# Kernel optimization log

Hardware: AMD Instinct MI355X
Metric: run time of the kernel (lower is better)

The kernel has to match this reference:

```python
import jax, jax.numpy as jnp
import numpy as np

EPS = 1e-6
B, N, WD, R = 64, 1024, 64, 4
IN_DIM, HID, OUT_DIM = 512, 512, 256


def oneplus(x):
    return 1.0 + jax.nn.softplus(x)


def content_weight(M, keys, strengths):
    # M:[B,N,W] keys:[B,R,W] strengths:[B,R] -> softmax over N -> [B,N,R]
    Mn = M * jax.lax.rsqrt(jnp.sum(M * M, -1, keepdims=True) + EPS)
    kn = keys * jax.lax.rsqrt(jnp.sum(keys * keys, -1, keepdims=True) + EPS)
    sim = jnp.einsum('bnw,brw->bnr', Mn, kn)
    return jax.nn.softmax(sim * strengths[:, None, :], axis=1)


def allocation(u):
    # DNC allocation weighting: sort usage ascending, exclusive cumprod, scatter back
    idx = jnp.argsort(u, axis=-1)
    us = jnp.take_along_axis(u, idx, -1)
    cp = jnp.cumprod(us, -1)
    cp_excl = jnp.concatenate([jnp.ones_like(cp[:, :1]), cp[:, :-1]], -1)
    a_sorted = (1.0 - us) * cp_excl
    inv = jnp.argsort(idx, axis=-1)
    return jnp.take_along_axis(a_sorted, inv, -1)


def setup_inputs() -> dict:
    key = jax.random.key(0)
    ks = jax.random.split(key, 16)
    rw = jax.random.uniform(ks[0], (B, N, R), dtype=jnp.float32)
    rw = rw / jnp.sum(rw, axis=1, keepdims=True)  # valid read distribution over N
    wwp = jax.random.uniform(ks[1], (B, N), dtype=jnp.float32)
    wwp = wwp / jnp.sum(wwp, axis=1, keepdims=True)
    s = 0.02
    return {
        'x': jax.random.normal(ks[2], (B, IN_DIM), dtype=jnp.float32),
        'read_weighting': rw,
        'memory': jax.random.normal(ks[3], (B, N, WD), dtype=jnp.float32) * 0.1,
        'usage': jax.random.uniform(ks[4], (B, N), dtype=jnp.float32),
        'write_weighting_prev': wwp,
        'link': jnp.zeros((B, N, N), dtype=jnp.float32),
        'precedence': jnp.zeros((B, N), dtype=jnp.float32),
        'W1': jax.random.normal(ks[5], (IN_DIM + R * WD, HID), dtype=jnp.float32) * s,
        'b1': jnp.zeros((HID,), dtype=jnp.float32),
        'Wo': jax.random.normal(ks[6], (HID, OUT_DIM), dtype=jnp.float32) * s,
        'bo': jnp.zeros((OUT_DIM,), dtype=jnp.float32),
        'Wr': jax.random.normal(ks[7], (R * WD, OUT_DIM), dtype=jnp.float32) * s,
        'br': jnp.zeros((OUT_DIM,), dtype=jnp.float32),
        'Wxi': jax.random.normal(ks[8], (HID, WD * R + 3 * WD + 5 * R + 3), dtype=jnp.float32) * s,
        'bxi': jnp.zeros((WD * R + 3 * WD + 5 * R + 3,), dtype=jnp.float32),
    }


def reference(x, read_weighting, memory, usage, write_weighting_prev, link, precedence,
              W1, b1, Wo, bo, Wr, br, Wxi, bxi):
    b, n, wd = memory.shape
    r = read_weighting.shape[-1]
    # --- read with incoming read weighting ---
    read_flat = jnp.einsum('bnw,bnr->brw', memory, read_weighting).reshape(b, r * wd)
    h = jax.nn.relu(jnp.concatenate([x, read_flat], -1) @ W1 + b1)
    output = (h @ Wo + bo) + (read_flat @ Wr + br)
    xi = h @ Wxi + bxi
    # --- interface split ---
    sizes = [wd * r, r, wd, 1, wd, wd, r, 1, 1, 3 * r]
    offs = np.cumsum([0] + sizes)
    p = [xi[:, offs[i]:offs[i + 1]] for i in range(10)]
    read_keys = p[0].reshape(b, r, wd)
    read_strengths = oneplus(p[1])
    write_key = p[2][:, None, :]
    write_strength = oneplus(p[3])
    erase = jax.nn.sigmoid(p[4])
    write_vec = p[5]
    free = jax.nn.sigmoid(p[6])
    ag = jax.nn.sigmoid(p[7])
    wg = jax.nn.sigmoid(p[8])
    read_modes = jax.nn.softmax(p[9].reshape(b, r, 3), axis=-1)
    # --- dynamic memory allocation ---
    retention = jnp.prod(1.0 - free[:, None, :] * read_weighting, axis=-1)  # [B,N]
    usage_new = (usage + write_weighting_prev - usage * write_weighting_prev) * retention
    alloc = allocation(usage_new)
    wc = content_weight(memory, write_key, write_strength)[:, :, 0]
    ww = wg * (ag * alloc + (1.0 - ag) * wc)  # [B,N]
    # --- erase / write ---
    memory_new = memory * (1.0 - ww[:, :, None] * erase[:, None, :]) \
        + ww[:, :, None] * write_vec[:, None, :]
    # --- temporal link matrix ---
    prec_new = (1.0 - jnp.sum(ww, -1, keepdims=True)) * precedence + ww
    link_new = (1.0 - ww[:, :, None] - ww[:, None, :]) * link \
        + ww[:, :, None] * precedence[:, None, :]
    link_new = link_new * (1.0 - jnp.eye(n, dtype=link.dtype))
    fwd_w = jnp.einsum('bij,bjr->bir', link_new, read_weighting)
    bwd_w = jnp.einsum('bji,bjr->bir', link_new, read_weighting)
    # --- new read weighting ---
    cr = content_weight(memory_new, read_keys, read_strengths)
    rw_new = read_modes[:, None, :, 0] * bwd_w \
        + read_modes[:, None, :, 1] * cr \
        + read_modes[:, None, :, 2] * fwd_w
    return output, xi, rw_new, memory_new, usage_new
```

## Files before the change

### kernel.cpp

```cpp
#include <hip/hip_runtime.h>

#define NB 64
#define NN 1024
#define WDIM 64
#define RR 4
#define HID 512
#define XID 471
#define EPSF 1e-6f

#define O_OUT   0
#define O_XI    16384
#define O_RW    46528
#define O_MEM   308672
#define O_USAGE 4502976

#define WS_RFPART   0
#define WS_H        65536
#define WS_IFACE    98304
#define WS_ALLOC    129024
#define WS_WW       194560
#define WS_V        260096
#define WS_DIAG     784896
#define WS_ROWAB    850432
#define WS_COLPART  1899008
#define WS_EW       6093312
#define WS_SIMWE    6093568
#define WS_ERP      6159104
#define WS_ER       6160128
#define WS_STP      6422272

#define IF_KN     0
#define IF_WKN    256
#define IF_ERASE  320
#define IF_WVEC   384
#define IF_RSTR   448
#define IF_FREE   452
#define IF_WSTR   456
#define IF_AG     457
#define IF_WG     458
#define IF_MODES  460
#define IF_STRIDE 480

__device__ __forceinline__ float sigmoidf_(float x) { return 1.0f / (1.0f + expf(-x)); }
__device__ __forceinline__ float oneplusf_(float x) {
  return 1.0f + ((x > 20.0f) ? x : log1pf(expf(x)));
}

typedef const __attribute__((address_space(1))) void gas_void;
typedef __attribute__((address_space(3))) void las_void;
__device__ __forceinline__ void gl16(const float* g, float* l) {
  __builtin_amdgcn_global_load_lds((gas_void*)g, (las_void*)l, 16, 0, 0);
}

__global__ __launch_bounds__(1024) void k_read_flat(const float* __restrict__ mem,
                                                    const float* __restrict__ rw,
                                                    float* __restrict__ ws) {
  __shared__ float red[1024];
  const int q = blockIdx.x, b = blockIdx.y, t = threadIdx.x;
  const int rwi = t & 255;
  const int r = rwi >> 6, w = rwi & 63;
  const int ng = t >> 8;
  const int n0 = (q << 8) + (ng << 6);
  const float* M  = mem + ((size_t)(b << 10) + n0) * WDIM;
  const float* Rw = rw  + ((size_t)(b << 10) + n0) * RR;
  float a0 = 0.f, a1 = 0.f, a2 = 0.f, a3 = 0.f;
  for (int n = 0; n < 64; n += 4) {
    a0 += M[(n + 0) * WDIM + w] * Rw[(n + 0) * RR + r];
    a1 += M[(n + 1) * WDIM + w] * Rw[(n + 1) * RR + r];
    a2 += M[(n + 2) * WDIM + w] * Rw[(n + 2) * RR + r];
    a3 += M[(n + 3) * WDIM + w] * Rw[(n + 3) * RR + r];
  }
  red[t] = (a0 + a1) + (a2 + a3);
  __syncthreads();
  if (t < 256)
    ws[WS_RFPART + (((q << 6) + b) << 8) + t] =
        red[t] + red[t + 256] + red[t + 512] + red[t + 768];
}

__global__ __launch_bounds__(256) void k_h(const float* __restrict__ x,
                                           const float* __restrict__ W1,
                                           const float* __restrict__ b1,
                                           float* __restrict__ ws) {
  __shared__ float cat[768];
  const int ch = blockIdx.x, b = blockIdx.y, t = threadIdx.x;
  cat[t] = x[b * 512 + t];
  cat[256 + t] = x[b * 512 + 256 + t];
  {
    float s = 0.0f;
    #pragma unroll
    for (int q = 0; q < 4; ++q) s += ws[WS_RFPART + (((q << 6) + b) << 8) + t];
    cat[512 + t] = s;
  }
  __syncthreads();
  const int col = (ch << 8) + t;
  float a0 = 0.f, a1 = 0.f, a2 = 0.f, a3 = 0.f;
  #pragma unroll 4
  for (int k = 0; k < 768; k += 4) {
    a0 = fmaf(cat[k + 0], W1[(k + 0) * 512 + col], a0);
    a1 = fmaf(cat[k + 1], W1[(k + 1) * 512 + col], a1);
    a2 = fmaf(cat[k + 2], W1[(k + 2) * 512 + col], a2);
    a3 = fmaf(cat[k + 3], W1[(k + 3) * 512 + col], a3);
  }
  ws[WS_H + b * 512 + col] = fmaxf(b1[col] + (a0 + a1) + (a2 + a3), 0.0f);
}

__global__ __launch_bounds__(256) void k_xiout(const float* __restrict__ Wxi,
                                               const float* __restrict__ bxi,
                                               const float* __restrict__ Wo,
                                               const float* __restrict__ bo,
                                               const float* __restrict__ Wr,
                                               const float* __restrict__ br,
                                               const float* __restrict__ ws,
                                               float* __restrict__ out) {
  __shared__ float h[512];
  __shared__ float rf[256];
  const int m = blockIdx.x, b = blockIdx.y, t = threadIdx.x;
  h[t] = ws[WS_H + b * 512 + t];
  h[256 + t] = ws[WS_H + b * 512 + 256 + t];
  if (m == 2) {
    float s = 0.0f;
    #pragma unroll
    for (int q = 0; q < 4; ++q) s += ws[WS_RFPART + (((q << 6) + b) << 8) + t];
    rf[t] = s;
  }
  __syncthreads();
  if (m < 2) {
    const int col = (m << 8) + t;
    if (col < XID) {
      float a0 = 0.f, a1 = 0.f, a2 = 0.f, a3 = 0.f;
      #pragma unroll 4
      for (int j = 0; j < 512; j += 4) {
        a0 = fmaf(h[j + 0], Wxi[(j + 0) * XID + col], a0);
        a1 = fmaf(h[j + 1], Wxi[(j + 1) * XID + col], a1);
        a2 = fmaf(h[j + 2], Wxi[(j + 2) * XID + col], a2);
        a3 = fmaf(h[j + 3], Wxi[(j + 3) * XID + col], a3);
      }
      out[O_XI + b * XID + col] = bxi[col] + (a0 + a1) + (a2 + a3);
    }
  } else {
    float a0 = 0.f, a1 = 0.f, a2 = 0.f, a3 = 0.f;
    #pragma unroll 4
    for (int j = 0; j < 512; j += 4) {
      a0 = fmaf(h[j + 0], Wo[(j + 0) * 256 + t], a0);
      a1 = fmaf(h[j + 1], Wo[(j + 1) * 256 + t], a1);
      a2 = fmaf(h[j + 2], Wo[(j + 2) * 256 + t], a2);
      a3 = fmaf(h[j + 3], Wo[(j + 3) * 256 + t], a3);
    }
    #pragma unroll 4
    for (int j = 0; j < 256; j += 4) {
      a0 = fmaf(rf[j + 0], Wr[(j + 0) * 256 + t], a0);
      a1 = fmaf(rf[j + 1], Wr[(j + 1) * 256 + t], a1);
      a2 = fmaf(rf[j + 2], Wr[(j + 2) * 256 + t], a2);
      a3 = fmaf(rf[j + 3], Wr[(j + 3) * 256 + t], a3);
    }
    out[O_OUT + b * 256 + t] = bo[t] + br[t] + (a0 + a1) + (a2 + a3);
  }
}

__global__ __launch_bounds__(64) void k_iface(const float* __restrict__ out,
                                              float* __restrict__ ws) {
  const int b = blockIdx.x, w = threadIdx.x;
  const float* xi = out + O_XI + b * XID;
  float* f = ws + WS_IFACE + (size_t)b * IF_STRIDE;
  #pragma unroll
  for (int r = 0; r < 4; ++r) {
    float kv = xi[r * 64 + w];
    float ss = kv * kv;
    #pragma unroll
    for (int s = 32; s; s >>= 1) ss += __shfl_xor(ss, s);
    f[IF_KN + r * 64 + w] = kv * rsqrtf(ss + EPSF);
  }
  {
    float kv = xi[260 + w];
    float ss = kv * kv;
    #pragma unroll
    for (int s = 32; s; s >>= 1) ss += __shfl_xor(ss, s);
    f[IF_WKN + w] = kv * rsqrtf(ss + EPSF);
  }
  f[IF_ERASE + w] = sigmoidf_(xi[325 + w]);
  f[IF_WVEC + w] = xi[389 + w];
  if (w < 4) {
    f[IF_RSTR + w] = oneplusf_(xi[256 + w]);
    f[IF_FREE + w] = sigmoidf_(xi[453 + w]);
    float a = xi[459 + w * 3], bb = xi[459 + w * 3 + 1], c = xi[459 + w * 3 + 2];
    float m = fmaxf(a, fmaxf(bb, c));
    float ea = expf(a - m), eb = expf(bb - m), ec = expf(c - m);
    float s = ea + eb + ec;
    f[IF_MODES + w * 3] = ea / s;
    f[IF_MODES + w * 3 + 1] = eb / s;
    f[IF_MODES + w * 3 + 2] = ec / s;
  }
  if (w == 0) {
    f[IF_WSTR] = oneplusf_(xi[324]);
    f[IF_AG] = sigmoidf_(xi[457]);
    f[IF_WG] = sigmoidf_(xi[458]);
  }
}

__global__ __launch_bounds__(256) void k_alloc(const float* __restrict__ rw,
                                               const float* __restrict__ usage,
                                               const float* __restrict__ wwp,
                                               float* __restrict__ ws,
                                               float* __restrict__ ousage) {
  __shared__ float2 ul[1024];
  const int q = blockIdx.x, b = blockIdx.y, t = threadIdx.x;
  const float* fr = ws + WS_IFACE + (size_t)b * IF_STRIDE + IF_FREE;
  const float f0 = fr[0], f1 = fr[1], f2 = fr[2], f3 = fr[3];
  #pragma unroll
  for (int c = 0; c < 4; ++c) {
    const int n = (c << 8) + t;
    const int i = (b << 10) + n;
    const float4 r4 = *(const float4*)(rw + (size_t)i * 4);
    float ret = (1.0f - f0 * r4.x) * (1.0f - f1 * r4.y) *
                (1.0f - f2 * r4.z) * (1.0f - f3 * r4.w);
    float u = usage[i], w = wwp[i];
    float un = (u + w - u * w) * ret;
    if (c == q) ousage[i] = un;
    ul[n] = make_float2(un, logf(un));
  }
  __syncthreads();
  const int i = (q << 8) + t;
  const float ui = ul[i].x;
  float s0 = 0.f, s1 = 0.f, s2 = 0.f, s3 = 0.f;
  #pragma unroll 2
  for (int j = 0; j < 1024; j += 4) {
    float2 v0 = ul[j], v1 = ul[j + 1], v2 = ul[j + 2], v3 = ul[j + 3];
    s0 += ((v0.x < ui) || (v0.x == ui && j + 0 < i)) ? v0.y : 0.0f;
    s1 += ((v1.x < ui) || (v1.x == ui && j + 1 < i)) ? v1.y : 0.0f;
    s2 += ((v2.x < ui) || (v2.x == ui && j + 2 < i)) ? v2.y : 0.0f;
    s3 += ((v3.x < ui) || (v3.x == ui && j + 3 < i)) ? v3.y : 0.0f;
  }
  ws[WS_ALLOC + (b << 10) + i] = (1.0f - ui) * expf((s0 + s1) + (s2 + s3));
}

__global__ __launch_bounds__(256) void k_wcww_a(const float* __restrict__ mem,
                                                const float* __restrict__ link,
                                                float* __restrict__ ws) {
  __shared__ float wkn[64];
  __shared__ float red[4];
  const int q = blockIdx.x, b = blockIdx.y, t = threadIdx.x;
  const int wv = t >> 6, lane = t & 63;
  const float* f = ws + WS_IFACE + (size_t)b * IF_STRIDE;
  if (t < 64) wkn[t] = f[IF_WKN + t];
  __syncthreads();
  const int n = (q << 8) + t;
  const size_t bn = (size_t)(b << 10) + n;
  const float* Mrow = mem + bn * WDIM;
  float dot = 0.0f, ssq = 0.0f;
  #pragma unroll
  for (int w = 0; w < 64; w += 4) {
    float4 m4 = *(const float4*)(Mrow + w);
    float4 k4 = *(const float4*)(&wkn[w]);
    dot += m4.x * k4.x + m4.y * k4.y + m4.z * k4.z + m4.w * k4.w;
    ssq += m4.x * m4.x + m4.y * m4.y + m4.z * m4.z + m4.w * m4.w;
  }
  float e = expf(dot * rsqrtf(ssq + EPSF) * f[IF_WSTR]);
  ws[WS_SIMWE + bn] = e;
  ws[WS_DIAG + bn] = link[bn * 1024 + n];
  float se = e;
  #pragma unroll
  for (int s = 32; s; s >>= 1) se += __shfl_xor(se, s);
  if (lane == 0) red[wv] = se;
  __syncthreads();
  if (t == 0) ws[WS_EW + (q << 6) + b] = red[0] + red[1] + red[2] + red[3];
}

__global__ __launch_bounds__(256) void k_wcww_b(const float* __restrict__ mem,
                                                const float* __restrict__ rw,
                                                const float* __restrict__ prec,
                                                float* __restrict__ ws,
                                                float* __restrict__ omem) {
  __shared__ float kn[256];
  __shared__ float shev[128];
  __shared__ float red8[4][8];
  __shared__ float red4[4][4];
  const int q = blockIdx.x, b = blockIdx.y, t = threadIdx.x;
  const int wv = t >> 6, lane = t & 63;
  const float* f = ws + WS_IFACE + (size_t)b * IF_STRIDE;
  kn[t] = f[IF_KN + t];
  if (t < 64) shev[t] = f[IF_ERASE + t];
  else if (t < 128) shev[t] = f[IF_WVEC + (t - 64)];
  __syncthreads();
  const float denom = ws[WS_EW + b] + ws[WS_EW + 64 + b] +
                      ws[WS_EW + 128 + b] + ws[WS_EW + 192 + b];
  const int n = (q << 8) + t;
  const size_t bn = (size_t)(b << 10) + n;
  float wc = ws[WS_SIMWE + bn] / denom;
  float ag = f[IF_AG], wg = f[IF_WG];
  float ww = wg * (ag * ws[WS_ALLOC + bn] + (1.0f - ag) * wc);
  ws[WS_WW + bn] = ww;
  float4 r4 = *(const float4*)(rw + bn * 4);
  float* vp = ws + WS_V + bn * 8;
  float4 v0 = {r4.x, r4.y, r4.z, r4.w};
  float4 v1 = {ww * r4.x, ww * r4.y, ww * r4.z, ww * r4.w};
  *(float4*)vp = v0;
  *(float4*)(vp + 4) = v1;
  float p = prec[bn];
  float vals[8] = {p * r4.x, p * r4.y, p * r4.z, p * r4.w,
                   ww * r4.x, ww * r4.y, ww * r4.z, ww * r4.w};
  #pragma unroll
  for (int k = 0; k < 8; ++k) {
    float v = vals[k];
    #pragma unroll
    for (int s = 32; s; s >>= 1) v += __shfl_xor(v, s);
    vals[k] = v;
  }
  if (lane == 0) {
    #pragma unroll
    for (int k = 0; k < 8; ++k) red8[wv][k] = vals[k];
  }
  const float* Mrow = mem + bn * WDIM;
  float* Orow = omem + bn * WDIM;
  float dr0 = 0.f, dr1 = 0.f, dr2 = 0.f, dr3 = 0.f, ssqn = 0.f;
  #pragma unroll
  for (int w4 = 0; w4 < 16; ++w4) {
    float4 m4 = *(const float4*)(Mrow + (w4 << 2));
    float4 e4 = *(const float4*)(&shev[w4 << 2]);
    float4 wv4 = *(const float4*)(&shev[64 + (w4 << 2)]);
    float4 o;
    o.x = m4.x * (1.0f - ww * e4.x) + ww * wv4.x;
    o.y = m4.y * (1.0f - ww * e4.y) + ww * wv4.y;
    o.z = m4.z * (1.0f - ww * e4.z) + ww * wv4.z;
    o.w = m4.w * (1.0f - ww * e4.w) + ww * wv4.w;
    *(float4*)(Orow + (w4 << 2)) = o;
    ssqn += o.x * o.x + o.y * o.y + o.z * o.z + o.w * o.w;
    float4 k0 = *(const float4*)(&kn[w4 << 2]);
    float4 k1 = *(const float4*)(&kn[64 + (w4 << 2)]);
    float4 k2 = *(const float4*)(&kn[128 + (w4 << 2)]);
    float4 k3 = *(const float4*)(&kn[192 + (w4 << 2)]);
    dr0 += o.x * k0.x + o.y * k0.y + o.z * k0.z + o.w * k0.w;
    dr1 += o.x * k1.x + o.y * k1.y + o.z * k1.z + o.w * k1.w;
    dr2 += o.x * k2.x + o.y * k2.y + o.z * k2.z + o.w * k2.w;
    dr3 += o.x * k3.x + o.y * k3.y + o.z * k3.z + o.w * k3.w;
  }
  float rs = rsqrtf(ssqn + EPSF);
  float er[4] = {expf(dr0 * rs * f[IF_RSTR + 0]), expf(dr1 * rs * f[IF_RSTR + 1]),
                 expf(dr2 * rs * f[IF_RSTR + 2]), expf(dr3 * rs * f[IF_RSTR + 3])};
  float4 er4 = {er[0], er[1], er[2], er[3]};
  *(float4*)(ws + WS_ER + bn * 4) = er4;
  #pragma unroll
  for (int r = 0; r < 4; ++r) {
    float v = er[r];
    #pragma unroll
    for (int s = 32; s; s >>= 1) v += __shfl_xor(v, s);
    er[r] = v;
  }
  if (lane == 0) {
    #pragma unroll
    for (int r = 0; r < 4; ++r) red4[wv][r] = er[r];
  }
  __syncthreads();
  if (t < 8)
    ws[WS_STP + (((q << 6) + b) << 3) + t] =
        red8[0][t] + red8[1][t] + red8[2][t] + red8[3][t];
  else if (t >= 64 && t < 68)
    ws[WS_ERP + (((q << 6) + b) << 2) + (t - 64)] =
        red4[0][t - 64] + red4[1][t - 64] + red4[2][t - 64] + red4[3][t - 64];
}

__global__ __launch_bounds__(512, 4) void k_link(const float* __restrict__ link,
                                                 float* __restrict__ ws) {
  __shared__ float buf[2][8192];
  __shared__ float vtile[2][512];
  __shared__ float ublk[1024];
  __shared__ float scr[1536];
  const int rg = blockIdx.x, b = blockIdx.y;
  const int wv = threadIdx.x >> 6, lane = threadIdx.x & 63;
  const int i0 = rg << 7;
  const int rot = ((rg << 1) + b) & 15;
  const float* L = link + ((size_t)b << 20) + ((size_t)i0 << 10);
  const float* V = ws + WS_V + ((size_t)b << 13);

  const float* gsrc[4];
  #pragma unroll
  for (int s = 0; s < 4; ++s) {
    const int qq = (wv << 2) + s;
    const int row = (qq << 2) + (lane >> 4);
    const int cb = (lane & 15) ^ (row & 15);
    gsrc[s] = L + (size_t)row * 1024 + (cb << 2);
  }

  float rowAcc[8], colAcc[8];
  #pragma unroll
  for (int k = 0; k < 8; ++k) { rowAcc[k] = 0.0f; colAcc[k] = 0.0f; }

  {
    const int c0 = rot << 6;
    #pragma unroll
    for (int s = 0; s < 4; ++s) gl16(gsrc[s] + c0, &buf[0][((wv << 2) + s) << 8]);
    if (wv < 2) gl16(V + ((size_t)c0 << 3) + (wv << 8) + (lane << 2), &vtile[0][wv << 8]);
    if (wv >= 4) gl16(V + ((size_t)(i0 + ((wv - 4) << 5)) << 3) + (lane << 2),
                      &ublk[(wv - 4) << 8]);
  }
  __syncthreads();

  int p = 0;
  #pragma unroll 1
  for (int jt = 0; jt < 16; ++jt) {
    const int jcur = ((jt + rot) & 15);
    if (jt < 15) {
      const int jn = ((jt + 1 + rot) & 15) << 6;
      #pragma unroll
      for (int s = 0; s < 4; ++s)
        gl16(gsrc[s] + jn, &buf[p ^ 1][((wv << 2) + s) << 8]);
      if (wv < 2) {
        gl16(V + ((size_t)jn << 3) + (wv << 8) + (lane << 2), &vtile[p ^ 1][wv << 8]);
        asm volatile("s_waitcnt vmcnt(5)" ::: "memory");
      } else {
        asm volatile("s_waitcnt vmcnt(4)" ::: "memory");
      }
    } else {
      asm volatile("s_waitcnt vmcnt(0)" ::: "memory");
    }
    __builtin_amdgcn_sched_barrier(0);
    __builtin_amdgcn_s_barrier();
    __builtin_amdgcn_sched_barrier(0);
    const float* tb = &buf[p][0];
    if (wv < 4) {
      const int rh = wv & 1, jh = wv >> 1;
      const int rr = (rh << 6) + lane;
      const float* base = tb + (rr << 6);
      const int rm = rr & 15;
      const float* vt = &vtile[p][0];
      #pragma unroll
      for (int jb8 = 0; jb8 < 8; ++jb8) {
        const int jb = (jh << 3) + jb8;
        float4 f4 = *(const float4*)(base + ((jb ^ rm) << 2));
        const float* vsb = vt + (jb << 5);
        #pragma unroll
        for (int q = 0; q < 4; ++q) {
          float fq = (q == 0) ? f4.x : (q == 1) ? f4.y : (q == 2) ? f4.z : f4.w;
          float4 a = *(const float4*)(vsb + (q << 3));
          float4 c = *(const float4*)(vsb + (q << 3) + 4);
          rowAcc[0] = fmaf(fq, a.x, rowAcc[0]);
          rowAcc[1] = fmaf(fq, a.y, rowAcc[1]);
          rowAcc[2] = fmaf(fq, a.z, rowAcc[2]);
          rowAcc[3] = fmaf(fq, a.w, rowAcc[3]);
          rowAcc[4] = fmaf(fq, c.x, rowAcc[4]);
          rowAcc[5] = fmaf(fq, c.y, rowAcc[5]);
          rowAcc[6] = fmaf(fq, c.z, rowAcc[6]);
          rowAcc[7] = fmaf(fq, c.w, rowAcc[7]);
        }
      }
    } else {
      const int iq = wv - 4;
      #pragma unroll 8
      for (int ii = 0; ii < 32; ++ii) {
        const int i = (iq << 5) + ii;
        float fq = tb[(i << 6) + ((((lane >> 2) ^ (i & 15)) << 2) | (lane & 3))];
        const float* ur = &ublk[i << 3];
        float4 a = *(const float4*)ur;
        float4 cc = *(const float4*)(ur + 4);
        colAcc[0] = fmaf(fq, a.x, colAcc[0]);
        colAcc[1] = fmaf(fq, a.y, colAcc[1]);
        colAcc[2] = fmaf(fq, a.z, colAcc[2]);
        colAcc[3] = fmaf(fq, a.w, colAcc[3]);
        colAcc[4] = fmaf(fq, cc.x, colAcc[4]);
        colAcc[5] = fmaf(fq, cc.y, colAcc[5]);
        colAcc[6] = fmaf(fq, cc.z, colAcc[6]);
        colAcc[7] = fmaf(fq, cc.w, colAcc[7]);
      }
      if (wv >= 5) {
        #pragma unroll
        for (int k = 0; k < 8; ++k)
          scr[((wv - 5) << 9) + (k << 6) + lane] = colAcc[k];
      }
    }
    asm volatile("s_waitcnt lgkmcnt(0)" ::: "memory");
    __builtin_amdgcn_s_barrier();
    __builtin_amdgcn_sched_barrier(0);
    if (wv == 4) {
      float* cp = ws + WS_COLPART + ((((size_t)rg << 6) + (size_t)b) << 13) +
                  (size_t)((jcur << 6) + lane) * 8;
      float s[8];
      #pragma unroll
      for (int k = 0; k < 8; ++k)
        s[k] = colAcc[k] + scr[(0 << 9) + (k << 6) + lane] +
               scr[(1 << 9) + (k << 6) + lane] +
               scr[(2 << 9) + (k << 6) + lane];
      float4 c0 = {s[0], s[1], s[2], s[3]};
      float4 c1 = {s[4], s[5], s[6], s[7]};
      *(float4*)cp = c0;
      *(float4*)(cp + 4) = c1;
    }
    if (wv >= 4) {
      #pragma unroll
      for (int k = 0; k < 8; ++k) colAcc[k] = 0.0f;
    }
    p ^= 1;
  }

  __syncthreads();
  if (wv == 2 || wv == 3) {
    #pragma unroll
    for (int k = 0; k < 8; ++k)
      buf[0][((wv & 1) << 9) + (lane << 3) + k] = rowAcc[k];
  }
  __syncthreads();
  if (wv < 2) {
    float* rp = ws + WS_ROWAB + ((size_t)(b << 10) + i0 + (wv << 6) + lane) * 8;
    #pragma unroll
    for (int k = 0; k < 8; ++k)
      rowAcc[k] += buf[0][(wv << 9) + (lane << 3) + k];
    float4 c0 = {rowAcc[0], rowAcc[1], rowAcc[2], rowAcc[3]};
    float4 c1 = {rowAcc[4], rowAcc[5], rowAcc[6], rowAcc[7]};
    *(float4*)rp = c0;
    *(float4*)(rp + 4) = c1;
  }
}

__global__ __launch_bounds__(256) void k_final(const float* __restrict__ rw,
                                               const float* __restrict__ prec,
                                               const float* __restrict__ ws,
                                               float* __restrict__ orw) {
  const int q = blockIdx.x, b = blockIdx.y, t = threadIdx.x;
  const float* f = ws + WS_IFACE + (size_t)b * IF_STRIDE;
  float denom[4], ST[8];
  #pragma unroll
  for (int r = 0; r < 4; ++r)
    denom[r] = ws[WS_ERP + (b << 2) + r] + ws[WS_ERP + ((64 + b) << 2) + r] +
               ws[WS_ERP + ((128 + b) << 2) + r] + ws[WS_ERP + ((192 + b) << 2) + r];
  #pragma unroll
  for (int k = 0; k < 8; ++k)
    ST[k] = ws[WS_STP + (b << 3) + k] + ws[WS_STP + ((64 + b) << 3) + k] +
            ws[WS_STP + ((128 + b) << 3) + k] + ws[WS_STP + ((192 + b) << 3) + k];
  const int n = (q << 8) + t;
  const size_t bn = (size_t)(b << 10) + n;
  float4 er4 = *(const float4*)(ws + WS_ER + bn * 4);
  float cr[4] = {er4.x / denom[0], er4.y / denom[1], er4.z / denom[2], er4.w / denom[3]};
  float ca[8];
  #pragma unroll
  for (int k = 0; k < 8; ++k) ca[k] = 0.0f;
  #pragma unroll
  for (int rg = 0; rg < 8; ++rg) {
    const float* p = ws + WS_COLPART + ((((size_t)rg << 6) + (size_t)b) << 13) +
                     (size_t)n * 8;
    float4 a = *(const float4*)p;
    float4 c2 = *(const float4*)(p + 4);
    ca[0] += a.x; ca[1] += a.y; ca[2] += a.z; ca[3] += a.w;
    ca[4] += c2.x; ca[5] += c2.y; ca[6] += c2.z; ca[7] += c2.w;
  }
  const float* ra = ws + WS_ROWAB + bn * 8;
  float d = ws[WS_DIAG + bn];
  float w_ = ws[WS_WW + bn];
  float pn = prec[bn];
  float4 r4 = *(const float4*)(rw + bn * 4);
  float rv[4] = {r4.x, r4.y, r4.z, r4.w};
  float ow = 1.0f - w_;
  float res[4];
  #pragma unroll
  for (int r = 0; r < 4; ++r) {
    float A = ra[r], Ap = ra[4 + r], Bv = ca[r], Bp = ca[4 + r];
    float fwd = ow * (A - d * rv[r]) - (Ap - w_ * d * rv[r]) + w_ * (ST[r] - pn * rv[r]);
    float bwd = ow * (Bv - d * rv[r]) - (Bp - w_ * d * rv[r]) + pn * (ST[4 + r] - w_ * rv[r]);
    res[r] = f[IF_MODES + r * 3] * bwd + f[IF_MODES + r * 3 + 1] * cr[r] +
             f[IF_MODES + r * 3 + 2] * fwd;
  }
  float4 o = {res[0], res[1], res[2], res[3]};
  *(float4*)(orw + bn * 4) = o;
}

extern "C" void kernel_launch(void* const* d_in, const int* in_sizes, int n_in,
                              void* d_out, int out_size, void* d_ws, size_t ws_size,
                              hipStream_t stream) {
  const float* x     = (const float*)d_in[0];
  const float* rw    = (const float*)d_in[1];
  const float* mem   = (const float*)d_in[2];
  const float* usage = (const float*)d_in[3];
  const float* wwp   = (const float*)d_in[4];
  const float* link  = (const float*)d_in[5];
  const float* prec  = (const float*)d_in[6];
  const float* W1    = (const float*)d_in[7];
  const float* b1    = (const float*)d_in[8];
  const float* Wo    = (const float*)d_in[9];
  const float* bo    = (const float*)d_in[10];
  const float* Wr    = (const float*)d_in[11];
  const float* br    = (const float*)d_in[12];
  const float* Wxi   = (const float*)d_in[13];
  const float* bxi   = (const float*)d_in[14];
  float* out = (float*)d_out;
  float* ws = (float*)d_ws;

  k_read_flat<<<dim3(4, 64), 1024, 0, stream>>>(mem, rw, ws);
  k_h<<<dim3(2, 64), 256, 0, stream>>>(x, W1, b1, ws);
  k_xiout<<<dim3(3, 64), 256, 0, stream>>>(Wxi, bxi, Wo, bo, Wr, br, ws, out);
  k_iface<<<64, 64, 0, stream>>>(out, ws);
  k_alloc<<<dim3(4, 64), 256, 0, stream>>>(rw, usage, wwp, ws, out + O_USAGE);
  k_wcww_a<<<dim3(4, 64), 256, 0, stream>>>(mem, link, ws);
  k_wcww_b<<<dim3(4, 64), 256, 0, stream>>>(mem, rw, prec, ws, out + O_MEM);
  k_link<<<dim3(8, 64), 512, 0, stream>>>(link, ws);
  k_final<<<dim3(4, 64), 256, 0, stream>>>(rw, prec, ws, out + O_RW);
}
```

Measured before the change: 242.4 us.

## Merge alloc and write-content kernels; halve link row-group size to double grid

Fuses the allocation kernel and the write-content-similarity kernel into one launch, with blocks selected by blockIdx.x, which removes one kernel launch. The link kernel now processes 64 rows per block with 256 threads instead of 128 rows with 512. That doubles the grid to 16 row groups and shrinks shared memory, aiming for better occupancy and load balance. The cost is twice as many column-partial buffers, so the workspace grows and k_final must sum 16 partials instead of 8.

```diff
diff --git a/kernel.cpp b/kernel.cpp
--- a/kernel.cpp
+++ b/kernel.cpp
@@ -23,11 +23,11 @@
 #define WS_DIAG     784896
 #define WS_ROWAB    850432
 #define WS_COLPART  1899008
-#define WS_EW       6093312
-#define WS_SIMWE    6093568
-#define WS_ERP      6159104
-#define WS_ER       6160128
-#define WS_STP      6422272
+#define WS_EW       10287616
+#define WS_SIMWE    10287872
+#define WS_ERP      10353408
+#define WS_ER       10354432
+#define WS_STP      10616576
 
 #define IF_KN     0
 #define IF_WKN    256
@@ -197,72 +197,73 @@
   }
 }
 
-__global__ __launch_bounds__(256) void k_alloc(const float* __restrict__ rw,
-                                               const float* __restrict__ usage,
-                                               const float* __restrict__ wwp,
-                                               float* __restrict__ ws,
-                                               float* __restrict__ ousage) {
+__global__ __launch_bounds__(256) void k_allocwc(const float* __restrict__ rw,
+                                                 const float* __restrict__ usage,
+                                                 const float* __restrict__ wwp,
+                                                 const float* __restrict__ mem,
+                                                 const float* __restrict__ link,
+                                                 float* __restrict__ ws,
+                                                 float* __restrict__ ousage) {
   __shared__ float2 ul[1024];
-  const int q = blockIdx.x, b = blockIdx.y, t = threadIdx.x;
-  const float* fr = ws + WS_IFACE + (size_t)b * IF_STRIDE + IF_FREE;
-  const float f0 = fr[0], f1 = fr[1], f2 = fr[2], f3 = fr[3];
-  #pragma unroll
-  for (int c = 0; c < 4; ++c) {
-    const int n = (c << 8) + t;
-    const int i = (b << 10) + n;
-    const float4 r4 = *(const float4*)(rw + (size_t)i * 4);
-    float ret = (1.0f - f0 * r4.x) * (1.0f - f1 * r4.y) *
-                (1.0f - f2 * r4.z) * (1.0f - f3 * r4.w);
-    float u = usage[i], w = wwp[i];
-    float un = (u + w - u * w) * ret;
-    if (c == q) ousage[i] = un;
-    ul[n] = make_float2(un, logf(un));
-  }
-  __syncthreads();
-  const int i = (q << 8) + t;
-  const float ui = ul[i].x;
-  float s0 = 0.f, s1 = 0.f, s2 = 0.f, s3 = 0.f;
-  #pragma unroll 2
-  for (int j = 0; j < 1024; j += 4) {
-    float2 v0 = ul[j], v1 = ul[j + 1], v2 = ul[j + 2], v3 = ul[j + 3];
-    s0 += ((v0.x < ui) || (v0.x == ui && j + 0 < i)) ? v0.y : 0.0f;
-    s1 += ((v1.x < ui) || (v1.x == ui && j + 1 < i)) ? v1.y : 0.0f;
-    s2 += ((v2.x < ui) || (v2.x == ui && j + 2 < i)) ? v2.y : 0.0f;
-    s3 += ((v3.x < ui) || (v3.x == ui && j + 3 < i)) ? v3.y : 0.0f;
-  }
-  ws[WS_ALLOC + (b << 10) + i] = (1.0f - ui) * expf((s0 + s1) + (s2 + s3));
-}
-
-__global__ __launch_bounds__(256) void k_wcww_a(const float* __restrict__ mem,
-                                                const float* __restrict__ link,
-                                                float* __restrict__ ws) {
   __shared__ float wkn[64];
   __shared__ float red[4];
-  const int q = blockIdx.x, b = blockIdx.y, t = threadIdx.x;
-  const int wv = t >> 6, lane = t & 63;
+  const int z = blockIdx.x, b = blockIdx.y, t = threadIdx.x;
   const float* f = ws + WS_IFACE + (size_t)b * IF_STRIDE;
-  if (t < 64) wkn[t] = f[IF_WKN + t];
-  __syncthreads();
-  const int n = (q << 8) + t;
-  const size_t bn = (size_t)(b << 10) + n;
-  const float* Mrow = mem + bn * WDIM;
-  float dot = 0.0f, ssq = 0.0f;
-  #pragma unroll
-  for (int w = 0; w < 64; w += 4) {
-    float4 m4 = *(const float4*)(Mrow + w);
-    float4 k4 = *(const float4*)(&wkn[w]);
-    dot += m4.x * k4.x + m4.y * k4.y + m4.z * k4.z + m4.w * k4.w;
-    ssq += m4.x * m4.x + m4.y * m4.y + m4.z * m4.z + m4.w * m4.w;
-  }
-  float e = expf(dot * rsqrtf(ssq + EPSF) * f[IF_WSTR]);
-  ws[WS_SIMWE + bn] = e;
-  ws[WS_DIAG + bn] = link[bn * 1024 + n];
-  float se = e;
-  #pragma unroll
-  for (int s = 32; s; s >>= 1) se += __shfl_xor(se, s);
-  if (lane == 0) red[wv] = se;
-  __syncthreads();
-  if (t == 0) ws[WS_EW + (q << 6) + b] = red[0] + red[1] + red[2] + red[3];
+  if (z < 4) {
+    const int q = z;
+    const float f0 = f[IF_FREE + 0], f1 = f[IF_FREE + 1];
+    const float f2 = f[IF_FREE + 2], f3 = f[IF_FREE + 3];
+    #pragma unroll
+    for (int c = 0; c < 4; ++c) {
+      const int n = (c << 8) + t;
+      const int i = (b << 10) + n;
+      const float4 r4 = *(const float4*)(rw + (size_t)i * 4);
+      float ret = (1.0f - f0 * r4.x) * (1.0f - f1 * r4.y) *
+                  (1.0f - f2 * r4.z) * (1.0f - f3 * r4.w);
+      float u = usage[i], w = wwp[i];
+      float un = (u + w - u * w) * ret;
+      if (c == q) ousage[i] = un;
+      ul[n] = make_float2(un, logf(un));
+    }
+    __syncthreads();
+    const int i = (q << 8) + t;
+    const float ui = ul[i].x;
+    float s0 = 0.f, s1 = 0.f, s2 = 0.f, s3 = 0.f;
+    #pragma unroll 2
+    for (int j = 0; j < 1024; j += 4) {
+      float2 v0 = ul[j], v1 = ul[j + 1], v2 = ul[j + 2], v3 = ul[j + 3];
+      s0 += ((v0.x < ui) || (v0.x == ui && j + 0 < i)) ? v0.y : 0.0f;
+      s1 += ((v1.x < ui) || (v1.x == ui && j + 1 < i)) ? v1.y : 0.0f;
+      s2 += ((v2.x < ui) || (v2.x == ui && j + 2 < i)) ? v2.y : 0.0f;
+      s3 += ((v3.x < ui) || (v3.x == ui && j + 3 < i)) ? v3.y : 0.0f;
+    }
+    ws[WS_ALLOC + (b << 10) + i] = (1.0f - ui) * expf((s0 + s1) + (s2 + s3));
+  } else {
+    const int q = z - 4;
+    const int wv = t >> 6, lane = t & 63;
+    if (t < 64) wkn[t] = f[IF_WKN + t];
+    __syncthreads();
+    const int n = (q << 8) + t;
+    const size_t bn = (size_t)(b << 10) + n;
+    const float* Mrow = mem + bn * WDIM;
+    float dot = 0.0f, ssq = 0.0f;
+    #pragma unroll
+    for (int w = 0; w < 64; w += 4) {
+      float4 m4 = *(const float4*)(Mrow + w);
+      float4 k4 = *(const float4*)(&wkn[w]);
+      dot += m4.x * k4.x + m4.y * k4.y + m4.z * k4.z + m4.w * k4.w;
+      ssq += m4.x * m4.x + m4.y * m4.y + m4.z * m4.z + m4.w * m4.w;
+    }
+    float e = expf(dot * rsqrtf(ssq + EPSF) * f[IF_WSTR]);
+    ws[WS_SIMWE + bn] = e;
+    ws[WS_DIAG + bn] = link[bn * 1024 + n];
+    float se = e;
+    #pragma unroll
+    for (int s = 32; s; s >>= 1) se += __shfl_xor(se, s);
+    if (lane == 0) red[wv] = se;
+    __syncthreads();
+    if (t == 0) ws[WS_EW + (q << 6) + b] = red[0] + red[1] + red[2] + red[3];
+  }
 }
 
 __global__ __launch_bounds__(256) void k_wcww_b(const float* __restrict__ mem,
@@ -358,15 +359,15 @@
         red4[0][t - 64] + red4[1][t - 64] + red4[2][t - 64] + red4[3][t - 64];
 }
 
-__global__ __launch_bounds__(512, 4) void k_link(const float* __restrict__ link,
+__global__ __launch_bounds__(256, 4) void k_link(const float* __restrict__ link,
                                                  float* __restrict__ ws) {
-  __shared__ float buf[2][8192];
+  __shared__ float buf[2][4096];
   __shared__ float vtile[2][512];
-  __shared__ float ublk[1024];
-  __shared__ float scr[1536];
+  __shared__ float ublk[512];
+  __shared__ float scr[512];
   const int rg = blockIdx.x, b = blockIdx.y;
   const int wv = threadIdx.x >> 6, lane = threadIdx.x & 63;
-  const int i0 = rg << 7;
+  const int i0 = rg << 6;
   const int rot = ((rg << 1) + b) & 15;
   const float* L = link + ((size_t)b << 20) + ((size_t)i0 << 10);
   const float* V = ws + WS_V + ((size_t)b << 13);
@@ -389,8 +390,8 @@
     #pragma unroll
     for (int s = 0; s < 4; ++s) gl16(gsrc[s] + c0, &buf[0][((wv << 2) + s) << 8]);
     if (wv < 2) gl16(V + ((size_t)c0 << 3) + (wv << 8) + (lane << 2), &vtile[0][wv << 8]);
-    if (wv >= 4) gl16(V + ((size_t)(i0 + ((wv - 4) << 5)) << 3) + (lane << 2),
-                      &ublk[(wv - 4) << 8]);
+    else        gl16(V + ((size_t)(i0 + ((wv - 2) << 5)) << 3) + (lane << 2),
+                     &ublk[(wv - 2) << 8]);
   }
   __syncthreads();
 
@@ -416,15 +417,13 @@
     __builtin_amdgcn_s_barrier();
     __builtin_amdgcn_sched_barrier(0);
     const float* tb = &buf[p][0];
-    if (wv < 4) {
-      const int rh = wv & 1, jh = wv >> 1;
-      const int rr = (rh << 6) + lane;
-      const float* base = tb + (rr << 6);
-      const int rm = rr & 15;
+    if (wv < 2) {
+      const float* base = tb + (lane << 6);
+      const int rm = lane & 15;
       const float* vt = &vtile[p][0];
       #pragma unroll
       for (int jb8 = 0; jb8 < 8; ++jb8) {
-        const int jb = (jh << 3) + jb8;
+        const int jb = (wv << 3) + jb8;
         float4 f4 = *(const float4*)(base + ((jb ^ rm) << 2));
         const float* vsb = vt + (jb << 5);
         #pragma unroll
@@ -443,7 +442,7 @@
         }
       }
     } else {
-      const int iq = wv - 4;
+      const int iq = wv - 2;
       #pragma unroll 8
       for (int ii = 0; ii < 32; ++ii) {
         const int i = (iq << 5) + ii;
@@ -460,30 +459,26 @@
         colAcc[6] = fmaf(fq, cc.z, colAcc[6]);
         colAcc[7] = fmaf(fq, cc.w, colAcc[7]);
       }
-      if (wv >= 5) {
+      if (wv == 3) {
         #pragma unroll
-        for (int k = 0; k < 8; ++k)
-          scr[((wv - 5) << 9) + (k << 6) + lane] = colAcc[k];
+        for (int k = 0; k < 8; ++k) scr[(k << 6) + lane] = colAcc[k];
       }
     }
     asm volatile("s_waitcnt lgkmcnt(0)" ::: "memory");
     __builtin_amdgcn_s_barrier();
     __builtin_amdgcn_sched_barrier(0);
-    if (wv == 4) {
+    if (wv == 2) {
       float* cp = ws + WS_COLPART + ((((size_t)rg << 6) + (size_t)b) << 13) +
                   (size_t)((jcur << 6) + lane) * 8;
       float s[8];
       #pragma unroll
-      for (int k = 0; k < 8; ++k)
-        s[k] = colAcc[k] + scr[(0 << 9) + (k << 6) + lane] +
-               scr[(1 << 9) + (k << 6) + lane] +
-               scr[(2 << 9) + (k << 6) + lane];
+      for (int k = 0; k < 8; ++k) s[k] = colAcc[k] + scr[(k << 6) + lane];
       float4 c0 = {s[0], s[1], s[2], s[3]};
       float4 c1 = {s[4], s[5], s[6], s[7]};
       *(float4*)cp = c0;
       *(float4*)(cp + 4) = c1;
     }
-    if (wv >= 4) {
+    if (wv >= 2) {
       #pragma unroll
       for (int k = 0; k < 8; ++k) colAcc[k] = 0.0f;
     }
@@ -491,17 +486,15 @@
   }
 
   __syncthreads();
-  if (wv == 2 || wv == 3) {
-    #pragma unroll
-    for (int k = 0; k < 8; ++k)
-      buf[0][((wv & 1) << 9) + (lane << 3) + k] = rowAcc[k];
-  }
-  __syncthreads();
-  if (wv < 2) {
-    float* rp = ws + WS_ROWAB + ((size_t)(b << 10) + i0 + (wv << 6) + lane) * 8;
-    #pragma unroll
-    for (int k = 0; k < 8; ++k)
-      rowAcc[k] += buf[0][(wv << 9) + (lane << 3) + k];
+  if (wv == 1) {
+    #pragma unroll
+    for (int k = 0; k < 8; ++k) buf[0][(lane << 3) + k] = rowAcc[k];
+  }
+  __syncthreads();
+  if (wv == 0) {
+    float* rp = ws + WS_ROWAB + ((size_t)(b << 10) + i0 + lane) * 8;
+    #pragma unroll
+    for (int k = 0; k < 8; ++k) rowAcc[k] += buf[0][(lane << 3) + k];
     float4 c0 = {rowAcc[0], rowAcc[1], rowAcc[2], rowAcc[3]};
     float4 c1 = {rowAcc[4], rowAcc[5], rowAcc[6], rowAcc[7]};
     *(float4*)rp = c0;
@@ -532,7 +525,7 @@
   #pragma unroll
   for (int k = 0; k < 8; ++k) ca[k] = 0.0f;
   #pragma unroll
-  for (int rg = 0; rg < 8; ++rg) {
+  for (int rg = 0; rg < 16; ++rg) {
     const float* p = ws + WS_COLPART + ((((size_t)rg << 6) + (size_t)b) << 13) +
                      (size_t)n * 8;
     float4 a = *(const float4*)p;
@@ -585,9 +578,8 @@
   k_h<<<dim3(2, 64), 256, 0, stream>>>(x, W1, b1, ws);
   k_xiout<<<dim3(3, 64), 256, 0, stream>>>(Wxi, bxi, Wo, bo, Wr, br, ws, out);
   k_iface<<<64, 64, 0, stream>>>(out, ws);
-  k_alloc<<<dim3(4, 64), 256, 0, stream>>>(rw, usage, wwp, ws, out + O_USAGE);
-  k_wcww_a<<<dim3(4, 64), 256, 0, stream>>>(mem, link, ws);
+  k_allocwc<<<dim3(8, 64), 256, 0, stream>>>(rw, usage, wwp, mem, link, ws, out + O_USAGE);
   k_wcww_b<<<dim3(4, 64), 256, 0, stream>>>(mem, rw, prec, ws, out + O_MEM);
-  k_link<<<dim3(8, 64), 512, 0, stream>>>(link, ws);
+  k_link<<<dim3(16, 64), 256, 0, stream>>>(link, ws);
   k_final<<<dim3(4, 64), 256, 0, stream>>>(rw, prec, ws, out + O_RW);
 }
```

After: 241.3 us. About the same (-0.5%).
